# Optimization experiments

Hardware: AMD Instinct MI355X
Metric: run time of the kernel (lower is better)

## Reference

```python
import jax, jax.numpy as jnp
import numpy as np

N = 50000
E = 600000
F_IN = 128
DIM = 128
BN_EPS = 1e-5


def _batchnorm(x, gamma, beta):
    # training-mode BatchNorm1d: biased batch stats over node dim
    mean = jnp.mean(x, axis=0)
    var = jnp.var(x, axis=0)
    return (x - mean) * jax.lax.rsqrt(var + BN_EPS) * gamma + beta


def _gin_layer(x, src, dst, Wa, ba, Wb, bb):
    # GINConv with eps=0: h_i = MLP(x_i + sum_{j->i} x_j)
    agg = jax.ops.segment_sum(x[src], dst, num_segments=N)
    h = x + agg
    h = jnp.maximum(h @ Wa + ba, 0.0) @ Wb + bb
    return h


def setup_inputs() -> dict:
    key = jax.random.key(0)
    ks = jax.random.split(key, 16)

    def lin(k, fan_in, fan_out):
        bound = 1.0 / np.sqrt(fan_in)
        kw, kb = jax.random.split(k)
        W = jax.random.uniform(kw, (fan_in, fan_out), jnp.float32, -bound, bound)
        b = jax.random.uniform(kb, (fan_out,), jnp.float32, -bound, bound)
        return W, b

    x = jax.random.normal(ks[0], (N, F_IN), jnp.float32)
    edge_index = jax.random.randint(ks[1], (2, E), 0, N, jnp.int64)

    W1a, b1a = lin(ks[2], F_IN, DIM)
    W1b, b1b = lin(ks[3], DIM, DIM)
    W2a, b2a = lin(ks[4], DIM, DIM)
    W2b, b2b = lin(ks[5], DIM, DIM)
    W5a, b5a = lin(ks[6], DIM, DIM)
    W5b, b5b = lin(ks[7], DIM, 2)

    g1 = jnp.ones((DIM,), jnp.float32); be1 = jnp.zeros((DIM,), jnp.float32)
    g2 = jnp.ones((DIM,), jnp.float32); be2 = jnp.zeros((DIM,), jnp.float32)
    g5 = jnp.ones((2,), jnp.float32); be5 = jnp.zeros((2,), jnp.float32)

    return dict(x=x, edge_index=edge_index,
                W1a=W1a, b1a=b1a, W1b=W1b, b1b=b1b, g1=g1, be1=be1,
                W2a=W2a, b2a=b2a, W2b=W2b, b2b=b2b, g2=g2, be2=be2,
                W5a=W5a, b5a=b5a, W5b=W5b, b5b=b5b, g5=g5, be5=be5)


def reference(x, edge_index,
              W1a, b1a, W1b, b1b, g1, be1,
              W2a, b2a, W2b, b2b, g2, be2,
              W5a, b5a, W5b, b5b, g5, be5):
    src, dst = edge_index[0], edge_index[1]
    h = jnp.maximum(_gin_layer(x, src, dst, W1a, b1a, W1b, b1b), 0.0)
    h = _batchnorm(h, g1, be1)
    h = jnp.maximum(_gin_layer(h, src, dst, W2a, b2a, W2b, b2b), 0.0)
    h = _batchnorm(h, g2, be2)
    h = jnp.maximum(_gin_layer(h, src, dst, W5a, b5a, W5b, b5b), 0.0)
    h = _batchnorm(h, g5, be5)
    return h
```

## Files before the change

kernel.cpp:

```cpp
#include <hip/hip_runtime.h>


constexpr int Nn = 50000;
constexpr int Ne = 600000;

typedef __attribute__((ext_vector_type(8))) short short8;
typedef __attribute__((ext_vector_type(4))) float f32x4;

__device__ inline float bflo(uint u) { return __uint_as_float(u << 16); }
__device__ inline float bfhi(uint u) { return __uint_as_float(u & 0xffff0000u); }
__device__ inline ushort f2b(float f) {
  uint x = __float_as_uint(f);
  return (ushort)((x + 0x7fffu + ((x >> 16) & 1u)) >> 16);
}
__device__ inline uint pack2(float a, float b) {
  return (uint)f2b(a) | ((uint)f2b(b) << 16);
}

constexpr int CVT_B = (Nn * 32) / 256;
constexpr int PK_B = (5 * 2048) / 256;
constexpr int EH_B = (Ne + 255) / 256;
__global__ __launch_bounds__(256) void prep_all(
    const float4* __restrict__ x4, uint2* __restrict__ xb,
    const float* __restrict__ Wa, const float* __restrict__ Wb,
    const float* __restrict__ Wc, const float* __restrict__ Wd,
    const float* __restrict__ We, ushort* __restrict__ pw,
    const int* __restrict__ dst, int* __restrict__ rp) {
  int b = blockIdx.x;
  if (b < CVT_B) {
    int i = b * 256 + threadIdx.x;
    float4 v = x4[i];
    xb[i] = make_uint2(pack2(v.x, v.y), pack2(v.z, v.w));
  } else if (b < CVT_B + PK_B) {
    int t = (b - CVT_B) * 256 + threadIdx.x;
    int mat = t >> 11;
    int r = t & 2047;
    int lane = r & 63;
    int ktnt = r >> 6;
    int kt = ktnt & 3, nt = ktnt >> 2;
    const float* W = mat == 0 ? Wa : mat == 1 ? Wb : mat == 2 ? Wc : mat == 3 ? Wd : We;
    int c = nt * 16 + (lane & 15);
    int k0 = kt * 32 + 8 * (lane >> 4);
    ushort tmp[8];
#pragma unroll
    for (int j = 0; j < 8; j++) tmp[j] = f2b(W[(size_t)(k0 + j) * 128 + c]);
    *(uint4*)&pw[(size_t)mat * 16384 + r * 8] = *(uint4*)tmp;
  } else {
    int e = (b - CVT_B - PK_B) * 256 + threadIdx.x;
    if (e < Ne) atomicAdd(&rp[dst[e] + 1], 1);
  }
}

constexpr int SCAN_N = Nn + 1;
constexpr int SCAN_G = (SCAN_N + 1023) / 1024;

__global__ __launch_bounds__(1024) void scan_p1(int* __restrict__ rp,
                                                int* __restrict__ bsum) {
  __shared__ int wsum[16];
  __shared__ int wpre[16];
  int i = blockIdx.x * 1024 + threadIdx.x;
  int lane = threadIdx.x & 63, wv = threadIdx.x >> 6;
  int v = (i < SCAN_N) ? rp[i] : 0;
#pragma unroll
  for (int off = 1; off < 64; off <<= 1) {
    int t = __shfl_up(v, off);
    if (lane >= off) v += t;
  }
  if (lane == 63) wsum[wv] = v;
  __syncthreads();
  if (threadIdx.x == 0) {
    int acc = 0;
#pragma unroll
    for (int w = 0; w < 16; w++) {
      wpre[w] = acc;
      acc += wsum[w];
    }
    bsum[blockIdx.x] = acc;
  }
  __syncthreads();
  if (i < SCAN_N) rp[i] = v + wpre[wv];
}

__global__ void scan_p2(int* __restrict__ bsum) {
  if (threadIdx.x == 0 && blockIdx.x == 0) {
    int acc = 0;
    for (int b = 0; b < SCAN_G; b++) {
      int t = bsum[b];
      bsum[b] = acc;
      acc += t;
    }
  }
}

__global__ __launch_bounds__(1024) void scan_p3(int* __restrict__ rp,
                                                const int* __restrict__ bsum,
                                                int* __restrict__ cur) {
  int i = blockIdx.x * 1024 + threadIdx.x;
  if (i < SCAN_N) {
    int v = rp[i] + bsum[blockIdx.x];
    rp[i] = v;
    if (i < Nn) cur[i] = v;
  }
}

__global__ __launch_bounds__(256) void edge_fill(const int* __restrict__ src,
                                                 const int* __restrict__ dst,
                                                 int* __restrict__ cur,
                                                 int* __restrict__ cols) {
  int e = blockIdx.x * 256 + threadIdx.x;
  if (e < Ne) {
    int p = atomicAdd(&cur[dst[e]], 1);
    cols[p] = src[e];
  }
}

template <bool FOLD>
__global__ __launch_bounds__(256) void gather_bn(const uint* __restrict__ X,
                                                 const int* __restrict__ rp,
                                                 const int* __restrict__ cols,
                                                 const float* __restrict__ sums,
                                                 const float* __restrict__ gamma,
                                                 const float* __restrict__ beta,
                                                 uint* __restrict__ H) {
  int wid = (blockIdx.x * 256 + threadIdx.x) >> 6;
  if (wid >= Nn) return;
  int lane = threadIdx.x & 63;
  int f0 = lane * 2;
  float A0 = 1.f, A1 = 1.f, B0 = 0.f, B1 = 0.f;
  if (FOLD) {
    float m0 = sums[f0] * (1.f / Nn), m1 = sums[f0 + 1] * (1.f / Nn);
    float v0 = sums[128 + f0] * (1.f / Nn) - m0 * m0;
    float v1 = sums[128 + f0 + 1] * (1.f / Nn) - m1 * m1;
    A0 = rsqrtf(v0 + 1e-5f) * gamma[f0];
    A1 = rsqrtf(v1 + 1e-5f) * gamma[f0 + 1];
    B0 = beta[f0] - m0 * A0;
    B1 = beta[f0 + 1] - m1 * A1;
  }
  int p0 = __builtin_amdgcn_readfirstlane(rp[wid]);
  int p1 = __builtin_amdgcn_readfirstlane(rp[wid + 1]);
  uint su = X[(size_t)wid * 64 + lane];
  float ax = bflo(su), ay = bfhi(su);
  int p = p0;
  for (; p + 4 <= p1; p += 4) {
    int s0 = __builtin_amdgcn_readfirstlane(cols[p]);
    int s1 = __builtin_amdgcn_readfirstlane(cols[p + 1]);
    int s2 = __builtin_amdgcn_readfirstlane(cols[p + 2]);
    int s3 = __builtin_amdgcn_readfirstlane(cols[p + 3]);
    uint u0 = X[(size_t)s0 * 64 + lane];
    uint u1 = X[(size_t)s1 * 64 + lane];
    uint u2 = X[(size_t)s2 * 64 + lane];
    uint u3 = X[(size_t)s3 * 64 + lane];
    ax += bflo(u0) + bflo(u1) + bflo(u2) + bflo(u3);
    ay += bfhi(u0) + bfhi(u1) + bfhi(u2) + bfhi(u3);
  }
  for (; p < p1; ++p) {
    int s0 = __builtin_amdgcn_readfirstlane(cols[p]);
    uint u0 = X[(size_t)s0 * 64 + lane];
    ax += bflo(u0);
    ay += bfhi(u0);
  }
  float cnt = (float)(p1 - p0 + 1);
  float ox = FOLD ? A0 * ax + cnt * B0 : ax;
  float oy = FOLD ? A1 * ay + cnt * B1 : ay;
  H[(size_t)wid * 64 + lane] = pack2(ox, oy);
}

__global__ __launch_bounds__(256, 2) void gin_mlp(const ushort* __restrict__ A,
                                                  const short8* __restrict__ pWa,
                                                  const float* __restrict__ ba,
                                                  const short8* __restrict__ pWb,
                                                  const float* __restrict__ bb,
                                                  ushort* __restrict__ C,
                                                  float* __restrict__ stats) {
  __shared__ ushort T[64][136];
  __shared__ float sS[128], sQ[128];
  int tid = threadIdx.x;
  if (tid < 128) {
    sS[tid] = 0.f;
    sQ[tid] = 0.f;
  }
  int wv = tid >> 6, l = tid & 63, lr = l & 15, lg = l >> 4;
  int rowb = wv * 16 + lr;
  int row = blockIdx.x * 64 + rowb;
  bool ok = row < Nn;

  short8 w[8][4];
#pragma unroll
  for (int nt = 0; nt < 8; nt++)
#pragma unroll
    for (int kt = 0; kt < 4; kt++) w[nt][kt] = pWa[(nt * 4 + kt) * 64 + l];
  short8 afr[4];
#pragma unroll
  for (int kt = 0; kt < 4; kt++) {
    afr[kt] = short8{};
    if (ok) afr[kt] = *(const short8*)(A + (size_t)row * 128 + kt * 32 + lg * 8);
  }
  f32x4 acc[8];
#pragma unroll
  for (int nt = 0; nt < 8; nt++) {
    float4 bv = *(const float4*)&ba[nt * 16 + lg * 4];
    acc[nt][0] = bv.x; acc[nt][1] = bv.y; acc[nt][2] = bv.z; acc[nt][3] = bv.w;
  }
  __syncthreads();
#pragma unroll
  for (int kt = 0; kt < 4; kt++)
#pragma unroll
    for (int nt = 0; nt < 8; nt++)
      acc[nt] = __builtin_amdgcn_mfma_f32_16x16x32_bf16(w[nt][kt], afr[kt], acc[nt],
                                                        0, 0, 0);
#pragma unroll
  for (int nt = 0; nt < 8; nt++) {
    float v0 = fmaxf(acc[nt][0], 0.f), v1 = fmaxf(acc[nt][1], 0.f);
    float v2 = fmaxf(acc[nt][2], 0.f), v3 = fmaxf(acc[nt][3], 0.f);
    *(uint2*)&T[rowb][nt * 16 + lg * 4] = make_uint2(pack2(v0, v1), pack2(v2, v3));
  }
  __syncthreads();

  short8 w2[8][4];
#pragma unroll
  for (int nt = 0; nt < 8; nt++)
#pragma unroll
    for (int kt = 0; kt < 4; kt++) w2[nt][kt] = pWb[(nt * 4 + kt) * 64 + l];
  short8 tfr[4];
#pragma unroll
  for (int kt = 0; kt < 4; kt++) tfr[kt] = *(const short8*)&T[rowb][kt * 32 + lg * 8];
  f32x4 acc2[8];
#pragma unroll
  for (int nt = 0; nt < 8; nt++) {
    float4 bv = *(const float4*)&bb[nt * 16 + lg * 4];
    acc2[nt][0] = bv.x; acc2[nt][1] = bv.y; acc2[nt][2] = bv.z; acc2[nt][3] = bv.w;
  }
#pragma unroll
  for (int kt = 0; kt < 4; kt++)
#pragma unroll
    for (int nt = 0; nt < 8; nt++)
      acc2[nt] = __builtin_amdgcn_mfma_f32_16x16x32_bf16(w2[nt][kt], tfr[kt], acc2[nt],
                                                         0, 0, 0);

#pragma unroll
  for (int nt = 0; nt < 8; nt++) {
    float v[4];
#pragma unroll
    for (int r = 0; r < 4; r++) v[r] = fmaxf(acc2[nt][r], 0.f);
    if (ok)
      *(uint2*)&C[(size_t)row * 128 + nt * 16 + lg * 4] =
          make_uint2(pack2(v[0], v[1]), pack2(v[2], v[3]));
#pragma unroll
    for (int r = 0; r < 4; r++) {
      float s_ = ok ? v[r] : 0.f;
      float q_ = s_ * s_;
      s_ += __shfl_xor(s_, 1);  q_ += __shfl_xor(q_, 1);
      s_ += __shfl_xor(s_, 2);  q_ += __shfl_xor(q_, 2);
      s_ += __shfl_xor(s_, 4);  q_ += __shfl_xor(q_, 4);
      s_ += __shfl_xor(s_, 8);  q_ += __shfl_xor(q_, 8);
      if (lr == 0) {
        atomicAdd(&sS[nt * 16 + lg * 4 + r], s_);
        atomicAdd(&sQ[nt * 16 + lg * 4 + r], q_);
      }
    }
  }
  __syncthreads();
  if (tid < 128) {
    atomicAdd(&stats[tid], sS[tid]);
    atomicAdd(&stats[128 + tid], sQ[tid]);
  }
}

__global__ __launch_bounds__(256, 2) void gin_mlp_out(const ushort* __restrict__ A,
                                                      const short8* __restrict__ pWa,
                                                      const float* __restrict__ ba,
                                                      const float* __restrict__ W5b,
                                                      const float* __restrict__ b5b,
                                                      float* __restrict__ O,
                                                      float* __restrict__ st3) {
  __shared__ ushort T[64][136];
  __shared__ float Wc[256];
  __shared__ float red[4][4];
  int tid = threadIdx.x;
  Wc[tid] = W5b[tid];
  int wv = tid >> 6, l = tid & 63, lr = l & 15, lg = l >> 4;
  int rowb = wv * 16 + lr;
  int row = blockIdx.x * 64 + rowb;
  bool ok = row < Nn;

  short8 w[8][4];
#pragma unroll
  for (int nt = 0; nt < 8; nt++)
#pragma unroll
    for (int kt = 0; kt < 4; kt++) w[nt][kt] = pWa[(nt * 4 + kt) * 64 + l];
  short8 afr[4];
#pragma unroll
  for (int kt = 0; kt < 4; kt++) {
    afr[kt] = short8{};
    if (ok) afr[kt] = *(const short8*)(A + (size_t)row * 128 + kt * 32 + lg * 8);
  }
  f32x4 acc[8];
#pragma unroll
  for (int nt = 0; nt < 8; nt++) {
    float4 bv = *(const float4*)&ba[nt * 16 + lg * 4];
    acc[nt][0] = bv.x; acc[nt][1] = bv.y; acc[nt][2] = bv.z; acc[nt][3] = bv.w;
  }
  __syncthreads();
#pragma unroll
  for (int kt = 0; kt < 4; kt++)
#pragma unroll
    for (int nt = 0; nt < 8; nt++)
      acc[nt] = __builtin_amdgcn_mfma_f32_16x16x32_bf16(w[nt][kt], afr[kt], acc[nt],
                                                        0, 0, 0);
#pragma unroll
  for (int nt = 0; nt < 8; nt++) {
    float v0 = fmaxf(acc[nt][0], 0.f), v1 = fmaxf(acc[nt][1], 0.f);
    float v2 = fmaxf(acc[nt][2], 0.f), v3 = fmaxf(acc[nt][3], 0.f);
    *(uint2*)&T[rowb][nt * 16 + lg * 4] = make_uint2(pack2(v0, v1), pack2(v2, v3));
  }
  __syncthreads();

  float a0 = 0.f, a1 = 0.f;
  int ks = lg * 32;
#pragma unroll
  for (int q = 0; q < 4; q++) {
    uint4 u = *(const uint4*)&T[rowb][ks + q * 8];
    uint uu[4] = {u.x, u.y, u.z, u.w};
#pragma unroll
    for (int h = 0; h < 4; h++) {
      int k = ks + q * 8 + h * 2;
      float e0 = bflo(uu[h]), e1 = bfhi(uu[h]);
      a0 = fmaf(e0, Wc[k * 2 + 0], a0);
      a1 = fmaf(e0, Wc[k * 2 + 1], a1);
      a0 = fmaf(e1, Wc[k * 2 + 2], a0);
      a1 = fmaf(e1, Wc[k * 2 + 3], a1);
    }
  }
  a0 += __shfl_xor(a0, 16);
  a0 += __shfl_xor(a0, 32);
  a1 += __shfl_xor(a1, 16);
  a1 += __shfl_xor(a1, 32);

  float o0 = 0.f, o1 = 0.f;
  if (l < 16 && ok) {
    o0 = fmaxf(a0 + b5b[0], 0.f);
    o1 = fmaxf(a1 + b5b[1], 0.f);
    *(float2*)&O[(size_t)row * 2] = make_float2(o0, o1);
  }
  float q0 = o0 * o0, q1 = o1 * o1;
#pragma unroll
  for (int off = 1; off < 64; off <<= 1) {
    o0 += __shfl_xor(o0, off);
    q0 += __shfl_xor(q0, off);
    o1 += __shfl_xor(o1, off);
    q1 += __shfl_xor(q1, off);
  }
  if (l == 0) {
    red[wv][0] = o0; red[wv][1] = o1; red[wv][2] = q0; red[wv][3] = q1;
  }
  __syncthreads();
  if (tid < 4) {
    float t = red[0][tid] + red[1][tid] + red[2][tid] + red[3][tid];
    atomicAdd(&st3[tid], t);
  }
}

__global__ __launch_bounds__(256) void bn_apply2(const float* __restrict__ H,
                                                 const float* __restrict__ sums,
                                                 const float* __restrict__ gamma,
                                                 const float* __restrict__ beta,
                                                 float* __restrict__ Out, int nRows) {
  int idx = blockIdx.x * 256 + threadIdx.x;
  if (idx >= nRows * 2) return;
  int f = idx & 1;
  float mean = sums[f] * (1.0f / Nn);
  float var = sums[2 + f] * (1.0f / Nn) - mean * mean;
  float inv = rsqrtf(var + 1e-5f);
  Out[idx] = (H[idx] - mean) * inv * gamma[f] + beta[f];
}

extern "C" void kernel_launch(void* const* d_in, const int* in_sizes, int n_in,
                              void* d_out, int out_size, void* d_ws, size_t ws_size,
                              hipStream_t stream) {
  const float* x = (const float*)d_in[0];
  const int* src = (const int*)d_in[1];
  const int* dst = src + Ne;
  const float* W1a = (const float*)d_in[2];
  const float* b1a = (const float*)d_in[3];
  const float* W1b = (const float*)d_in[4];
  const float* b1b = (const float*)d_in[5];
  const float* g1 = (const float*)d_in[6];
  const float* be1 = (const float*)d_in[7];
  const float* W2a = (const float*)d_in[8];
  const float* b2a = (const float*)d_in[9];
  const float* W2b = (const float*)d_in[10];
  const float* b2b = (const float*)d_in[11];
  const float* g2 = (const float*)d_in[12];
  const float* be2 = (const float*)d_in[13];
  const float* W5a = (const float*)d_in[14];
  const float* b5a = (const float*)d_in[15];
  const float* W5b = (const float*)d_in[16];
  const float* b5b = (const float*)d_in[17];
  const float* g5 = (const float*)d_in[18];
  const float* be5 = (const float*)d_in[19];

  char* base = (char*)d_ws;
  size_t off = 0;
  auto carve = [&](size_t bytes) {
    char* p = base + off;
    off += (bytes + 255) & ~(size_t)255;
    return p;
  };
  float* stats = (float*)carve(520 * 4);
  float* o2buf = (float*)carve((size_t)Nn * 2 * 4);
  int* rowptr = (int*)carve((size_t)(Nn + 1) * 4);
  int* cur = (int*)carve((size_t)Nn * 4);
  int* cols = (int*)carve((size_t)Ne * 4);
  int* bsum = (int*)carve((size_t)SCAN_G * 4);
  ushort* xb = (ushort*)carve((size_t)Nn * 128 * 2);
  ushort* bufA = (ushort*)carve((size_t)Nn * 128 * 2);
  ushort* bufB = (ushort*)carve((size_t)Nn * 128 * 2);
  ushort* pw = (ushort*)carve((size_t)5 * 16384 * 2);
  float* st1 = stats, *st2 = stats + 256, *st3 = stats + 512;

  hipMemsetAsync(stats, 0, 520 * sizeof(float), stream);
  hipMemsetAsync(rowptr, 0, (Nn + 1) * sizeof(int), stream);

  const int eGrid = (Ne + 255) / 256;
  const int gatherGrid = (Nn * 64 + 255) / 256;
  const int mlpGrid = (Nn + 63) / 64;

  prep_all<<<CVT_B + PK_B + EH_B, 256, 0, stream>>>(
      (const float4*)x, (uint2*)xb, W1a, W1b, W2a, W2b, W5a, pw, dst, rowptr);
  scan_p1<<<SCAN_G, 1024, 0, stream>>>(rowptr, bsum);
  scan_p2<<<1, 64, 0, stream>>>(bsum);
  scan_p3<<<SCAN_G, 1024, 0, stream>>>(rowptr, bsum, cur);
  edge_fill<<<eGrid, 256, 0, stream>>>(src, dst, cur, cols);

  const short8* pW1a = (const short8*)pw;
  const short8* pW1b = (const short8*)(pw + 16384);
  const short8* pW2a = (const short8*)(pw + 32768);
  const short8* pW2b = (const short8*)(pw + 49152);
  const short8* pW5a = (const short8*)(pw + 65536);

  gather_bn<false><<<gatherGrid, 256, 0, stream>>>((const uint*)xb, rowptr, cols,
                                                   nullptr, nullptr, nullptr,
                                                   (uint*)bufA);
  gin_mlp<<<mlpGrid, 256, 0, stream>>>(bufA, pW1a, b1a, pW1b, b1b, bufB, st1);

  gather_bn<true><<<gatherGrid, 256, 0, stream>>>((const uint*)bufB, rowptr, cols, st1,
                                                  g1, be1, (uint*)bufA);
  gin_mlp<<<mlpGrid, 256, 0, stream>>>(bufA, pW2a, b2a, pW2b, b2b, bufB, st2);

  gather_bn<true><<<gatherGrid, 256, 0, stream>>>((const uint*)bufB, rowptr, cols, st2,
                                                  g2, be2, (uint*)bufA);
  gin_mlp_out<<<mlpGrid, 256, 0, stream>>>(bufA, pW5a, b5a, W5b, b5b, o2buf, st3);
  bn_apply2<<<(Nn * 2 + 255) / 256, 256, 0, stream>>>(o2buf, st3, g5, be5,
                                                      (float*)d_out, Nn);
}
```

Before: 258.9 us.

## Process multiple row tiles per MLP block to amortize weight loads

The gin_mlp and gin_mlp_out kernels now loop over four 64-row tiles per block, loading the packed weight fragments into registers once and reusing them across tiles. The second-layer weights are preloaded alongside the first. Per-block shared-memory and global stat atomics are also amortized. In exchange, register pressure rises (both weight sets live at once), the grid shrinks to about 196 blocks, which may underfill the GPU, and each tile adds extra barriers.

```diff
diff --git a/kernel.cpp b/kernel.cpp
--- a/kernel.cpp
+++ b/kernel.cpp
@@ -165,6 +165,7 @@
   H[(size_t)wid * 64 + lane] = pack2(ox, oy);
 }
 
+constexpr int MLP_ROWS = 256;
 __global__ __launch_bounds__(256, 2) void gin_mlp(const ushort* __restrict__ A,
                                                   const short8* __restrict__ pWa,
                                                   const float* __restrict__ ba,
@@ -181,85 +182,89 @@
   }
   int wv = tid >> 6, l = tid & 63, lr = l & 15, lg = l >> 4;
   int rowb = wv * 16 + lr;
-  int row = blockIdx.x * 64 + rowb;
-  bool ok = row < Nn;
-
-  short8 w[8][4];
+  int row0 = blockIdx.x * MLP_ROWS;
+
+  short8 w1r[8][4], w2r[8][4];
 #pragma unroll
   for (int nt = 0; nt < 8; nt++)
 #pragma unroll
-    for (int kt = 0; kt < 4; kt++) w[nt][kt] = pWa[(nt * 4 + kt) * 64 + l];
-  short8 afr[4];
-#pragma unroll
-  for (int kt = 0; kt < 4; kt++) {
-    afr[kt] = short8{};
-    if (ok) afr[kt] = *(const short8*)(A + (size_t)row * 128 + kt * 32 + lg * 8);
-  }
-  f32x4 acc[8];
-#pragma unroll
-  for (int nt = 0; nt < 8; nt++) {
-    float4 bv = *(const float4*)&ba[nt * 16 + lg * 4];
-    acc[nt][0] = bv.x; acc[nt][1] = bv.y; acc[nt][2] = bv.z; acc[nt][3] = bv.w;
-  }
+    for (int kt = 0; kt < 4; kt++) {
+      w1r[nt][kt] = pWa[(nt * 4 + kt) * 64 + l];
+      w2r[nt][kt] = pWb[(nt * 4 + kt) * 64 + l];
+    }
+  __builtin_amdgcn_sched_barrier(0);
   __syncthreads();
-#pragma unroll
-  for (int kt = 0; kt < 4; kt++)
-#pragma unroll
-    for (int nt = 0; nt < 8; nt++)
-      acc[nt] = __builtin_amdgcn_mfma_f32_16x16x32_bf16(w[nt][kt], afr[kt], acc[nt],
-                                                        0, 0, 0);
-#pragma unroll
-  for (int nt = 0; nt < 8; nt++) {
-    float v0 = fmaxf(acc[nt][0], 0.f), v1 = fmaxf(acc[nt][1], 0.f);
-    float v2 = fmaxf(acc[nt][2], 0.f), v3 = fmaxf(acc[nt][3], 0.f);
-    *(uint2*)&T[rowb][nt * 16 + lg * 4] = make_uint2(pack2(v0, v1), pack2(v2, v3));
-  }
-  __syncthreads();
-
-  short8 w2[8][4];
-#pragma unroll
-  for (int nt = 0; nt < 8; nt++)
-#pragma unroll
-    for (int kt = 0; kt < 4; kt++) w2[nt][kt] = pWb[(nt * 4 + kt) * 64 + l];
-  short8 tfr[4];
-#pragma unroll
-  for (int kt = 0; kt < 4; kt++) tfr[kt] = *(const short8*)&T[rowb][kt * 32 + lg * 8];
-  f32x4 acc2[8];
-#pragma unroll
-  for (int nt = 0; nt < 8; nt++) {
-    float4 bv = *(const float4*)&bb[nt * 16 + lg * 4];
-    acc2[nt][0] = bv.x; acc2[nt][1] = bv.y; acc2[nt][2] = bv.z; acc2[nt][3] = bv.w;
-  }
-#pragma unroll
-  for (int kt = 0; kt < 4; kt++)
-#pragma unroll
-    for (int nt = 0; nt < 8; nt++)
-      acc2[nt] = __builtin_amdgcn_mfma_f32_16x16x32_bf16(w2[nt][kt], tfr[kt], acc2[nt],
-                                                         0, 0, 0);
-
-#pragma unroll
-  for (int nt = 0; nt < 8; nt++) {
-    float v[4];
-#pragma unroll
-    for (int r = 0; r < 4; r++) v[r] = fmaxf(acc2[nt][r], 0.f);
-    if (ok)
-      *(uint2*)&C[(size_t)row * 128 + nt * 16 + lg * 4] =
-          make_uint2(pack2(v[0], v[1]), pack2(v[2], v[3]));
-#pragma unroll
-    for (int r = 0; r < 4; r++) {
-      float s_ = ok ? v[r] : 0.f;
-      float q_ = s_ * s_;
-      s_ += __shfl_xor(s_, 1);  q_ += __shfl_xor(q_, 1);
-      s_ += __shfl_xor(s_, 2);  q_ += __shfl_xor(q_, 2);
-      s_ += __shfl_xor(s_, 4);  q_ += __shfl_xor(q_, 4);
-      s_ += __shfl_xor(s_, 8);  q_ += __shfl_xor(q_, 8);
-      if (lr == 0) {
-        atomicAdd(&sS[nt * 16 + lg * 4 + r], s_);
-        atomicAdd(&sQ[nt * 16 + lg * 4 + r], q_);
+
+  for (int rt = 0; rt < MLP_ROWS / 64; rt++) {
+    int row = row0 + rt * 64 + rowb;
+    bool ok = row < Nn;
+
+    short8 afr[4];
+#pragma unroll
+    for (int kt = 0; kt < 4; kt++) {
+      afr[kt] = short8{};
+      if (ok) afr[kt] = *(const short8*)(A + (size_t)row * 128 + kt * 32 + lg * 8);
+    }
+    f32x4 acc[8];
+#pragma unroll
+    for (int nt = 0; nt < 8; nt++) {
+      float4 bv = *(const float4*)&ba[nt * 16 + lg * 4];
+      acc[nt][0] = bv.x; acc[nt][1] = bv.y; acc[nt][2] = bv.z; acc[nt][3] = bv.w;
+    }
+#pragma unroll
+    for (int kt = 0; kt < 4; kt++)
+#pragma unroll
+      for (int nt = 0; nt < 8; nt++)
+        acc[nt] = __builtin_amdgcn_mfma_f32_16x16x32_bf16(w1r[nt][kt], afr[kt],
+                                                          acc[nt], 0, 0, 0);
+#pragma unroll
+    for (int nt = 0; nt < 8; nt++) {
+      float v0 = fmaxf(acc[nt][0], 0.f), v1 = fmaxf(acc[nt][1], 0.f);
+      float v2 = fmaxf(acc[nt][2], 0.f), v3 = fmaxf(acc[nt][3], 0.f);
+      *(uint2*)&T[rowb][nt * 16 + lg * 4] = make_uint2(pack2(v0, v1), pack2(v2, v3));
+    }
+    __syncthreads();
+
+    short8 tfr[4];
+#pragma unroll
+    for (int kt = 0; kt < 4; kt++) tfr[kt] = *(const short8*)&T[rowb][kt * 32 + lg * 8];
+    f32x4 acc2[8];
+#pragma unroll
+    for (int nt = 0; nt < 8; nt++) {
+      float4 bv = *(const float4*)&bb[nt * 16 + lg * 4];
+      acc2[nt][0] = bv.x; acc2[nt][1] = bv.y; acc2[nt][2] = bv.z; acc2[nt][3] = bv.w;
+    }
+#pragma unroll
+    for (int kt = 0; kt < 4; kt++)
+#pragma unroll
+      for (int nt = 0; nt < 8; nt++)
+        acc2[nt] = __builtin_amdgcn_mfma_f32_16x16x32_bf16(w2r[nt][kt], tfr[kt],
+                                                           acc2[nt], 0, 0, 0);
+
+#pragma unroll
+    for (int nt = 0; nt < 8; nt++) {
+      float v[4];
+#pragma unroll
+      for (int r = 0; r < 4; r++) v[r] = fmaxf(acc2[nt][r], 0.f);
+      if (ok)
+        *(uint2*)&C[(size_t)row * 128 + nt * 16 + lg * 4] =
+            make_uint2(pack2(v[0], v[1]), pack2(v[2], v[3]));
+#pragma unroll
+      for (int r = 0; r < 4; r++) {
+        float s_ = ok ? v[r] : 0.f;
+        float q_ = s_ * s_;
+        s_ += __shfl_xor(s_, 1);  q_ += __shfl_xor(q_, 1);
+        s_ += __shfl_xor(s_, 2);  q_ += __shfl_xor(q_, 2);
+        s_ += __shfl_xor(s_, 4);  q_ += __shfl_xor(q_, 4);
+        s_ += __shfl_xor(s_, 8);  q_ += __shfl_xor(q_, 8);
+        if (lr == 0) {
+          atomicAdd(&sS[nt * 16 + lg * 4 + r], s_);
+          atomicAdd(&sQ[nt * 16 + lg * 4 + r], q_);
+        }
       }
     }
-  }
-  __syncthreads();
+    __syncthreads();
+  }
   if (tid < 128) {
     atomicAdd(&stats[tid], sS[tid]);
     atomicAdd(&stats[128 + tid], sQ[tid]);
@@ -280,78 +285,85 @@
   Wc[tid] = W5b[tid];
   int wv = tid >> 6, l = tid & 63, lr = l & 15, lg = l >> 4;
   int rowb = wv * 16 + lr;
-  int row = blockIdx.x * 64 + rowb;
-  bool ok = row < Nn;
+  int row0 = blockIdx.x * MLP_ROWS;
 
   short8 w[8][4];
 #pragma unroll
   for (int nt = 0; nt < 8; nt++)
 #pragma unroll
     for (int kt = 0; kt < 4; kt++) w[nt][kt] = pWa[(nt * 4 + kt) * 64 + l];
-  short8 afr[4];
-#pragma unroll
-  for (int kt = 0; kt < 4; kt++) {
-    afr[kt] = short8{};
-    if (ok) afr[kt] = *(const short8*)(A + (size_t)row * 128 + kt * 32 + lg * 8);
-  }
-  f32x4 acc[8];
-#pragma unroll
-  for (int nt = 0; nt < 8; nt++) {
-    float4 bv = *(const float4*)&ba[nt * 16 + lg * 4];
-    acc[nt][0] = bv.x; acc[nt][1] = bv.y; acc[nt][2] = bv.z; acc[nt][3] = bv.w;
-  }
+  __builtin_amdgcn_sched_barrier(0);
   __syncthreads();
-#pragma unroll
-  for (int kt = 0; kt < 4; kt++)
-#pragma unroll
-    for (int nt = 0; nt < 8; nt++)
-      acc[nt] = __builtin_amdgcn_mfma_f32_16x16x32_bf16(w[nt][kt], afr[kt], acc[nt],
-                                                        0, 0, 0);
-#pragma unroll
-  for (int nt = 0; nt < 8; nt++) {
-    float v0 = fmaxf(acc[nt][0], 0.f), v1 = fmaxf(acc[nt][1], 0.f);
-    float v2 = fmaxf(acc[nt][2], 0.f), v3 = fmaxf(acc[nt][3], 0.f);
-    *(uint2*)&T[rowb][nt * 16 + lg * 4] = make_uint2(pack2(v0, v1), pack2(v2, v3));
-  }
-  __syncthreads();
-
-  float a0 = 0.f, a1 = 0.f;
-  int ks = lg * 32;
-#pragma unroll
-  for (int q = 0; q < 4; q++) {
-    uint4 u = *(const uint4*)&T[rowb][ks + q * 8];
-    uint uu[4] = {u.x, u.y, u.z, u.w};
-#pragma unroll
-    for (int h = 0; h < 4; h++) {
-      int k = ks + q * 8 + h * 2;
-      float e0 = bflo(uu[h]), e1 = bfhi(uu[h]);
-      a0 = fmaf(e0, Wc[k * 2 + 0], a0);
-      a1 = fmaf(e0, Wc[k * 2 + 1], a1);
-      a0 = fmaf(e1, Wc[k * 2 + 2], a0);
-      a1 = fmaf(e1, Wc[k * 2 + 3], a1);
-    }
-  }
-  a0 += __shfl_xor(a0, 16);
-  a0 += __shfl_xor(a0, 32);
-  a1 += __shfl_xor(a1, 16);
-  a1 += __shfl_xor(a1, 32);
-
-  float o0 = 0.f, o1 = 0.f;
-  if (l < 16 && ok) {
-    o0 = fmaxf(a0 + b5b[0], 0.f);
-    o1 = fmaxf(a1 + b5b[1], 0.f);
-    *(float2*)&O[(size_t)row * 2] = make_float2(o0, o1);
-  }
-  float q0 = o0 * o0, q1 = o1 * o1;
+
+  float so0 = 0.f, so1 = 0.f, sq0 = 0.f, sq1 = 0.f;
+  for (int rt = 0; rt < MLP_ROWS / 64; rt++) {
+    int row = row0 + rt * 64 + rowb;
+    bool ok = row < Nn;
+
+    short8 afr[4];
+#pragma unroll
+    for (int kt = 0; kt < 4; kt++) {
+      afr[kt] = short8{};
+      if (ok) afr[kt] = *(const short8*)(A + (size_t)row * 128 + kt * 32 + lg * 8);
+    }
+    f32x4 acc[8];
+#pragma unroll
+    for (int nt = 0; nt < 8; nt++) {
+      float4 bv = *(const float4*)&ba[nt * 16 + lg * 4];
+      acc[nt][0] = bv.x; acc[nt][1] = bv.y; acc[nt][2] = bv.z; acc[nt][3] = bv.w;
+    }
+#pragma unroll
+    for (int kt = 0; kt < 4; kt++)
+#pragma unroll
+      for (int nt = 0; nt < 8; nt++)
+        acc[nt] = __builtin_amdgcn_mfma_f32_16x16x32_bf16(w[nt][kt], afr[kt], acc[nt],
+                                                          0, 0, 0);
+#pragma unroll
+    for (int nt = 0; nt < 8; nt++) {
+      float v0 = fmaxf(acc[nt][0], 0.f), v1 = fmaxf(acc[nt][1], 0.f);
+      float v2 = fmaxf(acc[nt][2], 0.f), v3 = fmaxf(acc[nt][3], 0.f);
+      *(uint2*)&T[rowb][nt * 16 + lg * 4] = make_uint2(pack2(v0, v1), pack2(v2, v3));
+    }
+    __syncthreads();
+
+    float a0 = 0.f, a1 = 0.f;
+    int ks = lg * 32;
+#pragma unroll
+    for (int q = 0; q < 4; q++) {
+      uint4 u = *(const uint4*)&T[rowb][ks + q * 8];
+      uint uu[4] = {u.x, u.y, u.z, u.w};
+#pragma unroll
+      for (int h = 0; h < 4; h++) {
+        int k = ks + q * 8 + h * 2;
+        float e0 = bflo(uu[h]), e1 = bfhi(uu[h]);
+        a0 = fmaf(e0, Wc[k * 2 + 0], a0);
+        a1 = fmaf(e0, Wc[k * 2 + 1], a1);
+        a0 = fmaf(e1, Wc[k * 2 + 2], a0);
+        a1 = fmaf(e1, Wc[k * 2 + 3], a1);
+      }
+    }
+    a0 += __shfl_xor(a0, 16);
+    a0 += __shfl_xor(a0, 32);
+    a1 += __shfl_xor(a1, 16);
+    a1 += __shfl_xor(a1, 32);
+    if (l < 16 && ok) {
+      float o0 = fmaxf(a0 + b5b[0], 0.f);
+      float o1 = fmaxf(a1 + b5b[1], 0.f);
+      *(float2*)&O[(size_t)row * 2] = make_float2(o0, o1);
+      so0 += o0; sq0 += o0 * o0;
+      so1 += o1; sq1 += o1 * o1;
+    }
+    __syncthreads();
+  }
 #pragma unroll
   for (int off = 1; off < 64; off <<= 1) {
-    o0 += __shfl_xor(o0, off);
-    q0 += __shfl_xor(q0, off);
-    o1 += __shfl_xor(o1, off);
-    q1 += __shfl_xor(q1, off);
+    so0 += __shfl_xor(so0, off);
+    sq0 += __shfl_xor(sq0, off);
+    so1 += __shfl_xor(so1, off);
+    sq1 += __shfl_xor(sq1, off);
   }
   if (l == 0) {
-    red[wv][0] = o0; red[wv][1] = o1; red[wv][2] = q0; red[wv][3] = q1;
+    red[wv][0] = so0; red[wv][1] = so1; red[wv][2] = sq0; red[wv][3] = sq1;
   }
   __syncthreads();
   if (tid < 4) {
@@ -423,7 +435,7 @@
 
   const int eGrid = (Ne + 255) / 256;
   const int gatherGrid = (Nn * 64 + 255) / 256;
-  const int mlpGrid = (Nn + 63) / 64;
+  const int mlpGrid = (Nn + MLP_ROWS - 1) / MLP_ROWS;
 
   prep_all<<<CVT_B + PK_B + EH_B, 256, 0, stream>>>(
       (const float4*)x, (uint2*)xb, W1a, W1b, W2a, W2b, W5a, pw, dst, rowptr);
```

Result: slower. 322.9 us (+24.7%).
